# Kernel tuning notes

Hardware: AMD Instinct MI355X
Metric: run time of the kernel (lower is better)

## Reference

```python
import jax, jax.numpy as jnp
import numpy as np

B, T, C = 4, 1024, 1024
H, G = 16, 1            # n_head, n_query_groups
D = C // H              # head_dim = 64
E, K = 4, 1             # moe_num_experts, moe_k
FF = 4 * C              # ffn/expert hidden = 4096
EPS = 1e-5


def setup_inputs() -> dict:
    key = jax.random.key(0)
    ks = jax.random.split(key, 24)
    w = lambda k, shape: (jax.random.normal(k, shape, jnp.float32) * 0.02)
    return {
        "x": jax.random.normal(ks[0], (B, T, C), jnp.float32),
        # attention (torch Linear weights stored as [in, out])
        "wq": w(ks[1], (C, C)), "wk": w(ks[2], (C, C)), "wv": w(ks[3], (C, C)),
        "wo": w(ks[4], (C, C)), "bo": jnp.zeros((C,), jnp.float32),
        # feedforward
        "ff_w1": w(ks[5], (C, FF)), "ff_b1": jnp.zeros((FF,), jnp.float32),
        "ff_w2": w(ks[6], (FF, C)), "ff_b2": jnp.zeros((C,), jnp.float32),
        # MoE experts (stacked) + gate
        "exp_w1": w(ks[7], (E, C, FF)), "exp_b1": jnp.zeros((E, FF), jnp.float32),
        "exp_w2": w(ks[8], (E, FF, C)), "exp_b2": jnp.zeros((E, C), jnp.float32),
        "gate_w": w(ks[9], (C, E)), "gate_b": jnp.zeros((E,), jnp.float32),
        # layernorms
        "ln1_g": jnp.ones((C,), jnp.float32), "ln1_b": jnp.zeros((C,), jnp.float32),
        "ln2_g": jnp.ones((C,), jnp.float32), "ln2_b": jnp.zeros((C,), jnp.float32),
        "ln3_g": jnp.ones((C,), jnp.float32), "ln3_b": jnp.zeros((C,), jnp.float32),
    }


def _ln(x, g, b):
    m = x.mean(-1, keepdims=True)
    v = x.var(-1, keepdims=True)
    return (x - m) / jnp.sqrt(v + EPS) * g + b


def reference(x, wq, wk, wv, wo, bo, ff_w1, ff_b1, ff_w2, ff_b2,
              exp_w1, exp_b1, exp_w2, exp_b2, gate_w, gate_b,
              ln1_g, ln1_b, ln2_g, ln2_b, ln3_g, ln3_b):
    Hg = H // G
    # ---- grouped-query causal self-attention ----
    h = _ln(x, ln1_g, ln1_b)
    # [B,T,C] -> [B,G,Hg,T,D]
    q = (h @ wq).reshape(B, T, G, Hg, D).transpose(0, 2, 3, 1, 4)
    k = (h @ wk).reshape(B, T, G, Hg, D).transpose(0, 2, 3, 1, 4)
    v = (h @ wv).reshape(B, T, G, Hg, D).transpose(0, 2, 3, 1, 4)
    scores = jnp.einsum('bghtd,bghsd->bghts', q, k) / np.float32(np.sqrt(D))
    causal = jnp.tril(jnp.ones((T, T), bool))
    scores = jnp.where(causal, scores, -jnp.inf)
    probs = jax.nn.softmax(scores, axis=-1)
    o = jnp.einsum('bghts,bghsd->bghtd', probs, v)          # [B,G,Hg,T,D]
    o = o.reshape(B, H, T, D).transpose(0, 2, 1, 3).reshape(B, T, C)
    x = x + o @ wo + bo
    # ---- dense feedforward ----
    h = _ln(x, ln2_g, ln2_b)
    x = x + jax.nn.relu(h @ ff_w1 + ff_b1) @ ff_w2 + ff_b2
    # ---- MoE: compute ALL experts densely, gather top-k (faithful to source) ----
    h = _ln(x, ln3_g, ln3_b)
    gate = h @ gate_w + gate_b                               # [B,T,E]
    topk_s, topk_i = jax.lax.top_k(gate, K)                  # [B,T,K]
    topk_w = jax.nn.softmax(topk_s, axis=-1)
    hidden = jax.nn.relu(jnp.einsum('btc,ech->bteh', h, exp_w1) + exp_b1)
    expert_out = jnp.einsum('bteh,ehc->btec', hidden, exp_w2) + exp_b2  # [B,T,E,C]
    sel = jnp.take_along_axis(expert_out, topk_i[..., None], axis=2)    # [B,T,K,C]
    moe = (sel * topk_w[..., None]).sum(axis=2)
    return x + moe
```

## Files before the change

kernel.cpp:

```cpp
#include <hip/hip_runtime.h>


using f16   = _Float16;
using f16x4 = __attribute__((ext_vector_type(4))) _Float16;
using f16x8 = __attribute__((ext_vector_type(8))) _Float16;
using f32x4 = __attribute__((ext_vector_type(4))) float;

__device__ __forceinline__ void async16(void* l, const void* g) {
  __builtin_amdgcn_global_load_lds(
      (const __attribute__((address_space(1))) unsigned*)g,
      (__attribute__((address_space(3))) unsigned*)l, 16, 0, 0);
}

template <bool SPLITW>
__global__ __launch_bounds__(256) void transpose_k(
    const float* __restrict__ in, f16* __restrict__ oh, f16* __restrict__ ol,
    int R, int Cc) {
  const size_t bofs = (size_t)blockIdx.y * R * Cc;
  in += bofs; oh += bofs;
  if constexpr (SPLITW) ol += bofs;
  __shared__ float tile[32][33];
  const int nbx = Cc >> 5;
  const int bx = blockIdx.x % nbx, by = blockIdx.x / nbx;
  const int tx = threadIdx.x & 31, ty = threadIdx.x >> 5;
#pragma unroll
  for (int i = 0; i < 4; ++i) {
    int r = ty + i * 8;
    tile[r][tx] = in[(size_t)(by * 32 + r) * Cc + bx * 32 + tx];
  }
  __syncthreads();
#pragma unroll
  for (int i = 0; i < 4; ++i) {
    int oc = ty + i * 8;
    float v = tile[tx][oc];
    size_t o = (size_t)(bx * 32 + oc) * R + by * 32 + tx;
    f16 hi = (f16)v;
    oh[o] = hi;
    if constexpr (SPLITW) ol[o] = (f16)(v - (float)hi);
  }
}

__global__ __launch_bounds__(256) void ln_k(
    const float* __restrict__ x, const float* __restrict__ g,
    const float* __restrict__ b, f16* __restrict__ outh, f16* __restrict__ outl) {
  const int row = blockIdx.x;
  const float4 vv = ((const float4*)(x + (size_t)row * 1024))[threadIdx.x];
  float s = vv.x + vv.y + vv.z + vv.w;
  float sq = vv.x * vv.x + vv.y * vv.y + vv.z * vv.z + vv.w * vv.w;
#pragma unroll
  for (int mm = 32; mm; mm >>= 1) { s += __shfl_xor(s, mm); sq += __shfl_xor(sq, mm); }
  __shared__ float red[8];
  const int wv = threadIdx.x >> 6;
  if ((threadIdx.x & 63) == 0) { red[wv] = s; red[4 + wv] = sq; }
  __syncthreads();
  s = red[0] + red[1] + red[2] + red[3];
  sq = red[4] + red[5] + red[6] + red[7];
  const float mean = s * 0.0009765625f;
  const float rstd = rsqrtf(sq * 0.0009765625f - mean * mean + 1e-5f);
  const int c = threadIdx.x * 4;
  const float xs[4] = {vv.x, vv.y, vv.z, vv.w};
  f16x4 ovh, ovl;
#pragma unroll
  for (int i = 0; i < 4; ++i) {
    float val = (xs[i] - mean) * rstd * g[c + i] + b[c + i];
    f16 hi = (f16)val;
    ovh[i] = hi;
    ovl[i] = (f16)(val - (float)hi);
  }
  *(f16x4*)(outh + (size_t)row * 1024 + c) = ovh;
  *(f16x4*)(outl + (size_t)row * 1024 + c) = ovl;
}

__global__ __launch_bounds__(256) void gate_k(
    const float* __restrict__ x, const float* __restrict__ g, const float* __restrict__ b,
    const float* __restrict__ gw, const float* __restrict__ gb,
    int* __restrict__ cnt, int* __restrict__ idxAll, int* __restrict__ eid) {
  const int t = blockIdx.x;
  const float4 vv = ((const float4*)(x + (size_t)t * 1024))[threadIdx.x];
  float s = vv.x + vv.y + vv.z + vv.w;
  float sq = vv.x * vv.x + vv.y * vv.y + vv.z * vv.z + vv.w * vv.w;
#pragma unroll
  for (int mm = 32; mm; mm >>= 1) { s += __shfl_xor(s, mm); sq += __shfl_xor(sq, mm); }
  __shared__ float red[8];
  __shared__ float redv[4][4];
  const int wv = threadIdx.x >> 6;
  if ((threadIdx.x & 63) == 0) { red[wv] = s; red[4 + wv] = sq; }
  __syncthreads();
  s = red[0] + red[1] + red[2] + red[3];
  sq = red[4] + red[5] + red[6] + red[7];
  const float mean = s * 0.0009765625f;
  const float rstd = rsqrtf(sq * 0.0009765625f - mean * mean + 1e-5f);
  const int c = threadIdx.x * 4;
  const float xs[4] = {vv.x, vv.y, vv.z, vv.w};
  float a0 = 0.f, a1 = 0.f, a2 = 0.f, a3 = 0.f;
#pragma unroll
  for (int i = 0; i < 4; ++i) {
    float ln = (xs[i] - mean) * rstd * g[c + i] + b[c + i];
    const float4 w4 = ((const float4*)gw)[c + i];
    a0 += ln * w4.x; a1 += ln * w4.y; a2 += ln * w4.z; a3 += ln * w4.w;
  }
#pragma unroll
  for (int mm = 32; mm; mm >>= 1) {
    a0 += __shfl_xor(a0, mm); a1 += __shfl_xor(a1, mm);
    a2 += __shfl_xor(a2, mm); a3 += __shfl_xor(a3, mm);
  }
  if ((threadIdx.x & 63) == 0) {
    redv[wv][0] = a0; redv[wv][1] = a1; redv[wv][2] = a2; redv[wv][3] = a3;
  }
  __syncthreads();
  if (threadIdx.x == 0) {
    float ge[4];
#pragma unroll
    for (int e = 0; e < 4; ++e)
      ge[e] = redv[0][e] + redv[1][e] + redv[2][e] + redv[3][e] + gb[e];
    int be = 0; float bvv = ge[0];
#pragma unroll
    for (int e = 1; e < 4; ++e) if (ge[e] > bvv) { bvv = ge[e]; be = e; }
    int pos = atomicAdd(&cnt[be], 1);
    idxAll[(be << 12) + pos] = t;
    eid[t] = be;
  }
}

__global__ void init_moe(int* cnt) { if (threadIdx.x < 4) cnt[threadIdx.x] = 0; }

#define MAXMT 36
__global__ void plan_k(const int* __restrict__ cnt, int* __restrict__ desc) {
  if (threadIdx.x == 0) {
    int t = 0;
    for (int e = 0; e < 4; ++e) {
      const int c = cnt[e];
      for (int m = 0; m < c; m += 128) desc[t++] = (e << 16) | (m >> 7);
    }
    for (; t < MAXMT; ++t) desc[t] = -1;
  }
}

template <bool MOE>
__global__ __launch_bounds__(256) void reduce_k(
    const float* __restrict__ p0, const float* __restrict__ p1,
    const float* __restrict__ res, const float* __restrict__ bias,
    const int* __restrict__ eid, float* __restrict__ o) {
  const int row = blockIdx.x, t = threadIdx.x;
  const float* bp = MOE ? bias + (size_t)eid[row] * 1024 : bias;
  const float4 a = ((const float4*)(p0 + (size_t)row * 1024))[t];
  const float4 b = ((const float4*)(p1 + (size_t)row * 1024))[t];
  const float4 r = ((const float4*)(res + (size_t)row * 1024))[t];
  const float4 bb = ((const float4*)bp)[t];
  float4 o4;
  o4.x = r.x + a.x + b.x + bb.x;
  o4.y = r.y + a.y + b.y + bb.y;
  o4.z = r.z + a.z + b.z + bb.z;
  o4.w = r.w + a.w + b.w + bb.w;
  ((float4*)(o + (size_t)row * 1024))[t] = o4;
}

template <bool SPLIT, bool RELU, bool BIAS, bool RES, bool GATHER, int OUT,
          bool QKV3, bool KSPLIT>
__global__ __launch_bounds__(256, SPLIT ? 2 : 3) void gemm_k(
    const f16* __restrict__ Ah, const f16* __restrict__ Al,
    const f16* __restrict__ Bh, const f16* __restrict__ Bl,
    float* __restrict__ outf, float* __restrict__ outf2,
    f16* __restrict__ outh, f16* __restrict__ outl,
    const float* __restrict__ bias, const float* __restrict__ res,
    const int* __restrict__ idxAll, const int* __restrict__ cntAll,
    const int* __restrict__ desc,
    int M, int N, int K) {
  const int NB = N >> 7;
  int m0, n0, ks = 0;
  int cnt = M;
  const int* idx = nullptr;
  if constexpr (GATHER) {
    int rem = blockIdx.x;
    if constexpr (KSPLIT) {
      const int half = (int)gridDim.x >> 1;
      ks = rem >= half; rem -= ks * half;
    }
    const int mt = rem / NB, nt = rem - mt * NB;
    const int d = desc[mt];
    if (d < 0) return;
    const int e = d >> 16;
    m0 = (d & 0xffff) << 7;
    n0 = nt << 7;
    cnt = cntAll[e];
    idx = idxAll + (e << 12);
    Bh += (size_t)e * N * K;
    if constexpr (SPLIT) Bl += (size_t)e * N * K;
    if (BIAS) bias += (size_t)e * N;
  } else {
    int rem = blockIdx.x;
    const int ntile = (int)gridDim.x >> (KSPLIT ? 1 : 0);
    if constexpr (KSPLIT) { ks = rem >= ntile; rem -= ks * ntile; }
    const int q2 = ntile >> 3;
    const int bid = (rem & 7) * q2 + (rem >> 3);
    m0 = (bid / NB) << 7; n0 = (bid % NB) << 7;
  }

  constexpr int RB = SPLIT ? 32768 : 16384;
  __shared__ __align__(16) char lds[SPLIT ? 65536 : 32768];

  const int tid = threadIdx.x;
  const int wave = tid >> 6, lane = tid & 63;
  const int wr = (wave >> 1) << 6, wc = (wave & 1) << 6;
  const int srow = lane >> 3;
  const int lc = (lane & 7) ^ srow;
  const int kofs = lc << 4;

  const int kshift = (KSPLIT && ks) ? (K >> 1) : 0;

  const char* sAh[4];
  const char* sAl[4];
  const char* sBh[4];
  const char* sBl[4];
#pragma unroll
  for (int s = 0; s < 4; ++s) {
    const int tr = (wave * 4 + s) * 8 + srow;
    int gm = m0 + tr;
    if constexpr (GATHER) gm = idx[gm < cnt ? gm : cnt - 1];
    sAh[s] = (const char*)Ah + ((size_t)gm * K + kshift) * 2 + kofs;
    sBh[s] = (const char*)Bh + ((size_t)(n0 + tr) * K + kshift) * 2 + kofs;
    if constexpr (SPLIT) {
      sAl[s] = (const char*)Al + ((size_t)gm * K + kshift) * 2 + kofs;
      sBl[s] = (const char*)Bl + ((size_t)(n0 + tr) * K + kshift) * 2 + kofs;
    }
  }
  char* const dstw = lds + wave * 4096;

  const int s4 = lane >> 4, l7 = lane & 7, fr = lane & 15;
  int rowA[4], colB[4];
#pragma unroll
  for (int i = 0; i < 4; ++i) rowA[i] = (wr + i * 16 + fr) * 128;
#pragma unroll
  for (int j = 0; j < 4; ++j) colB[j] = RB + (wc + j * 16 + fr) * 128;
  const int ch[2] = {((s4) ^ l7) << 4, ((4 + s4) ^ l7) << 4};

  f32x4 acc[4][4] = {};

  const int nt_ = (KSPLIT ? (K >> 1) : K) >> 6;

  for (int t = 0; t < nt_; ++t) {
    const size_t kb = (size_t)t << 7;
#pragma unroll
    for (int s = 0; s < 4; ++s) {
      async16(dstw + s * 1024, sAh[s] + kb);
      if constexpr (SPLIT) async16(dstw + 16384 + s * 1024, sAl[s] + kb);
      async16(dstw + RB + s * 1024, sBh[s] + kb);
      if constexpr (SPLIT) async16(dstw + RB + 16384 + s * 1024, sBl[s] + kb);
    }
    __syncthreads();
    __builtin_amdgcn_s_setprio(1);
#pragma unroll
    for (int kk = 0; kk < 2; ++kk) {
      f16x8 va[4], vb[4], va2[4], vb2[4];
#pragma unroll
      for (int i = 0; i < 4; ++i) {
        va[i] = *(const f16x8*)(lds + rowA[i] + ch[kk]);
        if constexpr (SPLIT) va2[i] = *(const f16x8*)(lds + 16384 + rowA[i] + ch[kk]);
      }
#pragma unroll
      for (int j = 0; j < 4; ++j) {
        vb[j] = *(const f16x8*)(lds + colB[j] + ch[kk]);
        if constexpr (SPLIT) vb2[j] = *(const f16x8*)(lds + 16384 + colB[j] + ch[kk]);
      }
#pragma unroll
      for (int i = 0; i < 4; ++i)
#pragma unroll
        for (int j = 0; j < 4; ++j) {
          acc[i][j] = __builtin_amdgcn_mfma_f32_16x16x32_f16(va[i], vb[j], acc[i][j], 0, 0, 0);
          if constexpr (SPLIT) {
            acc[i][j] = __builtin_amdgcn_mfma_f32_16x16x32_f16(va2[i], vb[j], acc[i][j], 0, 0, 0);
            acc[i][j] = __builtin_amdgcn_mfma_f32_16x16x32_f16(va[i], vb2[j], acc[i][j], 0, 0, 0);
          }
        }
    }
    __builtin_amdgcn_s_setprio(0);
    __syncthreads();
  }

  const int cl = lane & 15, rg = lane >> 4;
  float* const po = (OUT == 3) ? (ks ? outf2 : outf) : outf;
#pragma unroll
  for (int i = 0; i < 4; ++i) {
#pragma unroll
    for (int r = 0; r < 4; ++r) {
      const int mloc = m0 + wr + i * 16 + rg * 4 + r;
      if (GATHER && mloc >= cnt) continue;
      const int orow = GATHER ? idx[mloc] : mloc;
#pragma unroll
      for (int j = 0; j < 4; ++j) {
        const int col = n0 + wc + j * 16 + cl;
        float v2 = acc[i][j][r];
        if (BIAS) v2 += bias[col];
        if (RELU) v2 = v2 > 0.f ? v2 : 0.f;
        if (RES) v2 += res[(size_t)orow * N + col];
        size_t oidx;
        if constexpr (QKV3) {
          if (col < 2048) {
            oidx = ((size_t)(col >> 10) * M + orow) * 1024 + (col & 1023);
          } else {
            const int c = col - 2048;
            oidx = (size_t)2 * M * 1024 +
                   (((size_t)(orow >> 10) * 16 + (c >> 6)) * 64 + (c & 63)) * 1024 +
                   (orow & 1023);
          }
        } else {
          oidx = (size_t)orow * N + col;
        }
        if constexpr (OUT == 0 || OUT == 3) {
          po[oidx] = v2;
        } else if constexpr (OUT == 1) {
          f16 hi = (f16)v2;
          outh[oidx] = hi;
          outl[oidx] = (f16)(v2 - (float)hi);
        } else {
          outh[oidx] = (f16)v2;
        }
      }
    }
  }
}

__global__ __launch_bounds__(256, 3) void attn_k(
    const f16* __restrict__ qh, const f16* __restrict__ ql,
    const f16* __restrict__ kh, const f16* __restrict__ kl,
    const f16* __restrict__ vth, const f16* __restrict__ vtl,
    f16* __restrict__ oh, f16* __restrict__ ol) {
  const int qt = 15 - (blockIdx.x & 15), hd = (blockIdx.x >> 4) & 15, bb = blockIdx.x >> 8;
  const int tid = threadIdx.x, wave = tid >> 6, lane = tid & 63;
  __shared__ __align__(16) char QPs[16384], Ks[16384], Vs[16384];
  const int swz = (((lane & 7) ^ ((lane >> 3) & 7)) << 4);
  const size_t tok0 = (size_t)bb * 1024;
  const int hoff = hd * 64;
  const size_t vbase = ((size_t)(bb * 16 + hd) * 64) * 1024;
  const float L2E = 1.44269504089f;

#pragma unroll
  for (int r = 0; r < 2; ++r) {
    const int chunk = wave * 2 + r;
    const int row = chunk * 8 + (lane >> 3);
    const size_t byte = (((tok0 + qt * 64 + row) * 1024 + hoff) << 1) + swz;
    async16(QPs + chunk * 1024, (const char*)qh + byte);
    async16(QPs + 8192 + chunk * 1024, (const char*)ql + byte);
  }
  __syncthreads();
  f16x8 qr_h[2], qr_l[2];
#pragma unroll
  for (int ks = 0; ks < 2; ++ks) {
    const int qrow = wave * 16 + (lane & 15);
    const int qoff = qrow * 128 + ((((ks << 2) + (lane >> 4)) ^ (qrow & 7)) << 4);
    qr_h[ks] = *(const f16x8*)(QPs + qoff);
    qr_l[ks] = *(const f16x8*)(QPs + 8192 + qoff);
  }

  f32x4 oacc[4] = {};
  float mrun[4] = {-1e30f, -1e30f, -1e30f, -1e30f};
  float lrun[4] = {};

  for (int kt = 0; kt <= qt; ++kt) {
    __syncthreads();
#pragma unroll
    for (int r = 0; r < 2; ++r) {
      const int chunk = wave * 2 + r;
      const int row = chunk * 8 + (lane >> 3);
      const size_t kbyte = (((tok0 + kt * 64 + row) * 1024 + hoff) << 1) + swz;
      async16(Ks + chunk * 1024, (const char*)kh + kbyte);
      async16(Ks + 8192 + chunk * 1024, (const char*)kl + kbyte);
      const size_t vbyte = (((vbase + (size_t)row * 1024) + kt * 64) << 1) + swz;
      async16(Vs + chunk * 1024, (const char*)vth + vbyte);
      async16(Vs + 8192 + chunk * 1024, (const char*)vtl + vbyte);
    }
    __syncthreads();

    f32x4 s[4] = {};
#pragma unroll
    for (int ks = 0; ks < 2; ++ks) {
#pragma unroll
      for (int j = 0; j < 4; ++j) {
        const int col = j * 16 + (lane & 15);
        const int koff = col * 128 + ((((ks << 2) + (lane >> 4)) ^ (col & 7)) << 4);
        f16x8 b_h = *(const f16x8*)(Ks + koff);
        f16x8 b_l = *(const f16x8*)(Ks + 8192 + koff);
        s[j] = __builtin_amdgcn_mfma_f32_16x16x32_f16(qr_h[ks], b_h, s[j], 0, 0, 0);
        s[j] = __builtin_amdgcn_mfma_f32_16x16x32_f16(qr_l[ks], b_h, s[j], 0, 0, 0);
        s[j] = __builtin_amdgcn_mfma_f32_16x16x32_f16(qr_h[ks], b_l, s[j], 0, 0, 0);
      }
    }

    const bool diag = (kt == qt);
    float pmax[4] = {-1e30f, -1e30f, -1e30f, -1e30f};
#pragma unroll
    for (int j = 0; j < 4; ++j)
#pragma unroll
      for (int r = 0; r < 4; ++r) {
        float sv = s[j][r] * 0.125f;
        if (diag) {
          const int qloc = wave * 16 + (lane >> 4) * 4 + r;
          const int kvl = j * 16 + (lane & 15);
          if (kvl > qloc) sv = -1e30f;
        }
        s[j][r] = sv;
        pmax[r] = fmaxf(pmax[r], sv);
      }
    char* pbh = QPs + wave * 2048;
    char* pbl = QPs + 8192 + wave * 2048;
#pragma unroll
    for (int r = 0; r < 4; ++r) {
#pragma unroll
      for (int mm = 1; mm < 16; mm <<= 1)
        pmax[r] = fmaxf(pmax[r], __shfl_xor(pmax[r], mm, 16));
      const float mnew = fmaxf(mrun[r], pmax[r]);
      const float al = exp2f((mrun[r] - mnew) * L2E);
      mrun[r] = mnew;
      lrun[r] *= al;
      oacc[0][r] *= al; oacc[1][r] *= al; oacc[2][r] *= al; oacc[3][r] *= al;
    }

    float psum[4] = {};
#pragma unroll
    for (int j = 0; j < 4; ++j)
#pragma unroll
      for (int r = 0; r < 4; ++r) {
        const float p = exp2f((s[j][r] - mrun[r]) * L2E);
        psum[r] += p;
        const int lr = (lane >> 4) * 4 + r;
        const int kvl = j * 16 + (lane & 15);
        const int poff = lr * 128 + ((kvl * 2) ^ ((lr & 7) << 4));
        f16 ph = (f16)p;
        *(f16*)(pbh + poff) = ph;
        *(f16*)(pbl + poff) = (f16)(p - (float)ph);
      }
#pragma unroll
    for (int r = 0; r < 4; ++r) {
#pragma unroll
      for (int mm = 1; mm < 16; mm <<= 1)
        psum[r] += __shfl_xor(psum[r], mm, 16);
      lrun[r] += psum[r];
    }

#pragma unroll
    for (int ks = 0; ks < 2; ++ks) {
      const int prow = lane & 15;
      const int poff = prow * 128 + ((((ks << 2) + (lane >> 4)) ^ (prow & 7)) << 4);
      f16x8 a_h = *(const f16x8*)(pbh + poff);
      f16x8 a_l = *(const f16x8*)(pbl + poff);
#pragma unroll
      for (int jd = 0; jd < 4; ++jd) {
        const int col = jd * 16 + (lane & 15);
        const int voff = col * 128 + ((((ks << 2) + (lane >> 4)) ^ (col & 7)) << 4);
        f16x8 b_h = *(const f16x8*)(Vs + voff);
        f16x8 b_l = *(const f16x8*)(Vs + 8192 + voff);
        oacc[jd] = __builtin_amdgcn_mfma_f32_16x16x32_f16(a_h, b_h, oacc[jd], 0, 0, 0);
        oacc[jd] = __builtin_amdgcn_mfma_f32_16x16x32_f16(a_l, b_h, oacc[jd], 0, 0, 0);
        oacc[jd] = __builtin_amdgcn_mfma_f32_16x16x32_f16(a_h, b_l, oacc[jd], 0, 0, 0);
      }
    }
  }

#pragma unroll
  for (int r = 0; r < 4; ++r) {
    const float inv = 1.0f / lrun[r];
    const size_t trow = tok0 + qt * 64 + wave * 16 + (lane >> 4) * 4 + r;
#pragma unroll
    for (int jd = 0; jd < 4; ++jd) {
      const int col = hoff + jd * 16 + (lane & 15);
      const float val = oacc[jd][r] * inv;
      const f16 hi = (f16)val;
      oh[trow * 1024 + col] = hi;
      ol[trow * 1024 + col] = (f16)(val - (float)hi);
    }
  }
}

extern "C" void kernel_launch(void* const* d_in, const int* in_sizes, int n_in,
                              void* d_out, int out_size, void* d_ws, size_t ws_size,
                              hipStream_t stream) {
  const float* x0   = (const float*)d_in[0];
  const float* wq   = (const float*)d_in[1];
  const float* wk   = (const float*)d_in[2];
  const float* wv   = (const float*)d_in[3];
  const float* wo   = (const float*)d_in[4];
  const float* bo   = (const float*)d_in[5];
  const float* ffw1 = (const float*)d_in[6];
  const float* ffb1 = (const float*)d_in[7];
  const float* ffw2 = (const float*)d_in[8];
  const float* ffb2 = (const float*)d_in[9];
  const float* ew1  = (const float*)d_in[10];
  const float* eb1  = (const float*)d_in[11];
  const float* ew2  = (const float*)d_in[12];
  const float* eb2  = (const float*)d_in[13];
  const float* gw   = (const float*)d_in[14];
  const float* gb   = (const float*)d_in[15];
  const float* l1g  = (const float*)d_in[16];
  const float* l1b  = (const float*)d_in[17];
  const float* l2g  = (const float*)d_in[18];
  const float* l2b  = (const float*)d_in[19];
  const float* l3g  = (const float*)d_in[20];
  const float* l3b  = (const float*)d_in[21];
  float* out = (float*)d_out;

  char* w = (char*)d_ws;
  const size_t M1 = (size_t)1024 * 1024;
  const size_t A1 = (size_t)4096 * 1024 * 2;
  const size_t W4 = (size_t)1024 * 4096 * 2;
  f16* wqkvh = (f16*)w; w += 3 * M1 * 2;
  f16* wqkvl = (f16*)w; w += 3 * M1 * 2;
  f16* woh = (f16*)w; w += M1 * 2;
  f16* wol = (f16*)w; w += M1 * 2;
  f16* f1h = (f16*)w; w += W4;  f16* f1l = (f16*)w; w += W4;
  f16* f2h = (f16*)w; w += W4;  f16* f2l = (f16*)w; w += W4;
  f16* e1t = (f16*)w; w += 4 * W4;
  f16* e2t = (f16*)w; w += 4 * W4;
  f16* hh  = (f16*)w; w += A1;  f16* hl  = (f16*)w; w += A1;
  f16* qkv_h = (f16*)w; w += 3 * A1;
  f16* qkv_l = (f16*)w; w += 3 * A1;
  f16* o_h = (f16*)w; w += A1;  f16* o_l = (f16*)w; w += A1;
  float* x1 = (float*)w; w += (size_t)4096 * 1024 * 4;
  int* cnt = (int*)w; w += 256;
  int* idx = (int*)w; w += (size_t)4 * 4096 * 4;
  int* eid = (int*)w; w += (size_t)4096 * 4;
  int* desc = (int*)w; w += 256;
  f16* hid_h = qkv_h;
  f16* hid_l = (f16*)((char*)qkv_h + (((size_t)32) << 20));
  f16* ffh   = qkv_h;
  float* pW0 = (float*)hh;
  float* pW1 = (float*)qkv_h;
  float* pF0 = (float*)wqkvh;
  float* pF1 = (float*)hh;
  float* pM0 = (float*)((char*)qkv_l + (((size_t)8) << 20));
  float* pM1 = (float*)o_h;

  transpose_k<true><<<1024, 256, 0, stream>>>(wq, wqkvh, wqkvl, 1024, 1024);
  transpose_k<true><<<1024, 256, 0, stream>>>(wk, wqkvh + M1, wqkvl + M1, 1024, 1024);
  transpose_k<true><<<1024, 256, 0, stream>>>(wv, wqkvh + 2 * M1, wqkvl + 2 * M1, 1024, 1024);
  transpose_k<true><<<1024, 256, 0, stream>>>(wo, woh, wol, 1024, 1024);
  transpose_k<true><<<4096, 256, 0, stream>>>(ffw1, f1h, f1l, 1024, 4096);
  transpose_k<true><<<4096, 256, 0, stream>>>(ffw2, f2h, f2l, 4096, 1024);
  transpose_k<false><<<dim3(4096, 4), 256, 0, stream>>>(ew1, e1t, nullptr, 1024, 4096);
  transpose_k<false><<<dim3(4096, 4), 256, 0, stream>>>(ew2, e2t, nullptr, 4096, 1024);

  const size_t TOK = (size_t)4096 * 1024;
  ln_k<<<4096, 256, 0, stream>>>(x0, l1g, l1b, hh, hl);
  gemm_k<true, false, false, false, false, 1, true, false><<<768, 256, 0, stream>>>(
      hh, hl, wqkvh, wqkvl, nullptr, nullptr, qkv_h, qkv_l,
      nullptr, nullptr, nullptr, nullptr, nullptr, 4096, 3072, 1024);
  attn_k<<<1024, 256, 0, stream>>>(qkv_h, qkv_l, qkv_h + TOK, qkv_l + TOK,
                                   qkv_h + 2 * TOK, qkv_l + 2 * TOK, o_h, o_l);
  gemm_k<true, false, false, false, false, 3, false, true><<<512, 256, 0, stream>>>(
      o_h, o_l, woh, wol, pW0, pW1, nullptr, nullptr,
      nullptr, nullptr, nullptr, nullptr, nullptr, 4096, 1024, 1024);
  reduce_k<false><<<4096, 256, 0, stream>>>(pW0, pW1, x0, bo, nullptr, x1);

  ln_k<<<4096, 256, 0, stream>>>(x1, l2g, l2b, hh, hl);
  gemm_k<true, true, true, false, false, 1, false, false><<<1024, 256, 0, stream>>>(
      hh, hl, f1h, f1l, nullptr, nullptr, hid_h, hid_l,
      ffb1, nullptr, nullptr, nullptr, nullptr, 4096, 4096, 1024);
  gemm_k<true, false, false, false, false, 3, false, true><<<512, 256, 0, stream>>>(
      hid_h, hid_l, f2h, f2l, pF0, pF1, nullptr, nullptr,
      nullptr, nullptr, nullptr, nullptr, nullptr, 4096, 1024, 4096);
  reduce_k<false><<<4096, 256, 0, stream>>>(pF0, pF1, x1, ffb2, nullptr, out);

  ln_k<<<4096, 256, 0, stream>>>(out, l3g, l3b, hh, hl);
  init_moe<<<1, 64, 0, stream>>>(cnt);
  gate_k<<<4096, 256, 0, stream>>>(out, l3g, l3b, gw, gb, cnt, idx, eid);
  plan_k<<<1, 64, 0, stream>>>(cnt, desc);
  gemm_k<false, true, true, false, true, 2, false, false><<<MAXMT * 32, 256, 0, stream>>>(
      hh, nullptr, e1t, nullptr, nullptr, nullptr, ffh, nullptr,
      eb1, nullptr, idx, cnt, desc, 4096, 4096, 1024);
  gemm_k<false, false, false, false, true, 3, false, true><<<2 * MAXMT * 8, 256, 0, stream>>>(
      ffh, nullptr, e2t, nullptr, pM0, pM1, nullptr, nullptr,
      nullptr, nullptr, idx, cnt, desc, 4096, 1024, 4096);
  reduce_k<true><<<4096, 256, 0, stream>>>(pM0, pM1, out, eb2, eid, out);
}
```

Before: 730.9 us.

## Use 256x256 GEMM tiles with 512 threads, double-buffered LDS and 4-way K-split

Rewrites the GEMM kernel to use 256x256 output tiles computed by 8 waves. LDS is double-buffered (128KB), so the global-to-LDS load of the next K tile overlaps the MFMA work on the current one. The split-fp16 path becomes three sequential passes over K (hi*hi, lo*hi, hi*lo) instead of three interleaved MFMAs. Output-projection and down-projection GEMMs now split K four ways, with a wider reduce kernel summing four partials, and partial buffers are remapped onto scratch regions plus one new buffer. The intent is more data reuse per tile and better latency hiding, at the cost of one block per CU, fewer blocks in the grid, coarser MoE tile padding, and more partial-sum traffic.

```diff
diff --git a/kernel.cpp b/kernel.cpp
--- a/kernel.cpp
+++ b/kernel.cpp
@@ -124,13 +124,13 @@
 
 __global__ void init_moe(int* cnt) { if (threadIdx.x < 4) cnt[threadIdx.x] = 0; }
 
-#define MAXMT 36
+#define MAXMT 20
 __global__ void plan_k(const int* __restrict__ cnt, int* __restrict__ desc) {
   if (threadIdx.x == 0) {
     int t = 0;
     for (int e = 0; e < 4; ++e) {
       const int c = cnt[e];
-      for (int m = 0; m < c; m += 128) desc[t++] = (e << 16) | (m >> 7);
+      for (int m = 0; m < c; m += 256) desc[t++] = (e << 16) | (m >> 8);
     }
     for (; t < MAXMT; ++t) desc[t] = -1;
   }
@@ -139,49 +139,53 @@
 template <bool MOE>
 __global__ __launch_bounds__(256) void reduce_k(
     const float* __restrict__ p0, const float* __restrict__ p1,
+    const float* __restrict__ p2, const float* __restrict__ p3,
     const float* __restrict__ res, const float* __restrict__ bias,
     const int* __restrict__ eid, float* __restrict__ o) {
   const int row = blockIdx.x, t = threadIdx.x;
   const float* bp = MOE ? bias + (size_t)eid[row] * 1024 : bias;
   const float4 a = ((const float4*)(p0 + (size_t)row * 1024))[t];
   const float4 b = ((const float4*)(p1 + (size_t)row * 1024))[t];
+  const float4 c = ((const float4*)(p2 + (size_t)row * 1024))[t];
+  const float4 d = ((const float4*)(p3 + (size_t)row * 1024))[t];
   const float4 r = ((const float4*)(res + (size_t)row * 1024))[t];
   const float4 bb = ((const float4*)bp)[t];
   float4 o4;
-  o4.x = r.x + a.x + b.x + bb.x;
-  o4.y = r.y + a.y + b.y + bb.y;
-  o4.z = r.z + a.z + b.z + bb.z;
-  o4.w = r.w + a.w + b.w + bb.w;
+  o4.x = r.x + a.x + b.x + c.x + d.x + bb.x;
+  o4.y = r.y + a.y + b.y + c.y + d.y + bb.y;
+  o4.z = r.z + a.z + b.z + c.z + d.z + bb.z;
+  o4.w = r.w + a.w + b.w + c.w + d.w + bb.w;
   ((float4*)(o + (size_t)row * 1024))[t] = o4;
 }
 
 template <bool SPLIT, bool RELU, bool BIAS, bool RES, bool GATHER, int OUT,
-          bool QKV3, bool KSPLIT>
-__global__ __launch_bounds__(256, SPLIT ? 2 : 3) void gemm_k(
+          bool QKV3, int KS>
+__global__ __launch_bounds__(512, 1) void gemm_k(
     const f16* __restrict__ Ah, const f16* __restrict__ Al,
     const f16* __restrict__ Bh, const f16* __restrict__ Bl,
-    float* __restrict__ outf, float* __restrict__ outf2,
+    float* __restrict__ p0, float* __restrict__ p1,
+    float* __restrict__ p2, float* __restrict__ p3,
     f16* __restrict__ outh, f16* __restrict__ outl,
     const float* __restrict__ bias, const float* __restrict__ res,
     const int* __restrict__ idxAll, const int* __restrict__ cntAll,
     const int* __restrict__ desc,
     int M, int N, int K) {
-  const int NB = N >> 7;
+  const int NB = N >> 8;
   int m0, n0, ks = 0;
   int cnt = M;
   const int* idx = nullptr;
   if constexpr (GATHER) {
     int rem = blockIdx.x;
-    if constexpr (KSPLIT) {
-      const int half = (int)gridDim.x >> 1;
-      ks = rem >= half; rem -= ks * half;
+    if constexpr (KS > 1) {
+      const int per = (int)gridDim.x / KS;
+      ks = rem / per; rem -= ks * per;
     }
     const int mt = rem / NB, nt = rem - mt * NB;
     const int d = desc[mt];
     if (d < 0) return;
     const int e = d >> 16;
-    m0 = (d & 0xffff) << 7;
-    n0 = nt << 7;
+    m0 = (d & 0xffff) << 8;
+    n0 = nt << 8;
     cnt = cntAll[e];
     idx = idxAll + (e << 12);
     Bh += (size_t)e * N * K;
@@ -189,106 +193,118 @@
     if (BIAS) bias += (size_t)e * N;
   } else {
     int rem = blockIdx.x;
-    const int ntile = (int)gridDim.x >> (KSPLIT ? 1 : 0);
-    if constexpr (KSPLIT) { ks = rem >= ntile; rem -= ks * ntile; }
-    const int q2 = ntile >> 3;
-    const int bid = (rem & 7) * q2 + (rem >> 3);
-    m0 = (bid / NB) << 7; n0 = (bid % NB) << 7;
-  }
-
-  constexpr int RB = SPLIT ? 32768 : 16384;
-  __shared__ __align__(16) char lds[SPLIT ? 65536 : 32768];
+    const int ntile = (int)gridDim.x / KS;
+    if constexpr (KS > 1) { ks = rem / ntile; rem -= ks * ntile; }
+    const int q = ntile >> 3;
+    const int bid = (rem & 7) * q + (rem >> 3);
+    m0 = (bid / NB) << 8; n0 = (bid % NB) << 8;
+  }
+
+  __shared__ __align__(16) char lds[131072];
 
   const int tid = threadIdx.x;
   const int wave = tid >> 6, lane = tid & 63;
-  const int wr = (wave >> 1) << 6, wc = (wave & 1) << 6;
-  const int srow = lane >> 3;
-  const int lc = (lane & 7) ^ srow;
-  const int kofs = lc << 4;
-
-  const int kshift = (KSPLIT && ks) ? (K >> 1) : 0;
-
-  const char* sAh[4];
-  const char* sAl[4];
-  const char* sBh[4];
-  const char* sBl[4];
+  const int wm = wave >> 2, wn = wave & 3;
+  const int srow = lane >> 3, l7 = lane & 7;
+  const int kofs = (l7 ^ srow) << 4;
+
+  const int Kp = K / KS;
+  const int kshift = ks * Kp;
+  const int ntk = Kp >> 6;
+  const int nt = SPLIT ? 3 * ntk : ntk;
+
+  unsigned offA[4], offB[4];
 #pragma unroll
   for (int s = 0; s < 4; ++s) {
-    const int tr = (wave * 4 + s) * 8 + srow;
-    int gm = m0 + tr;
+    const int ar = wave * 32 + s * 8 + srow;
+    int gm = m0 + ar;
     if constexpr (GATHER) gm = idx[gm < cnt ? gm : cnt - 1];
-    sAh[s] = (const char*)Ah + ((size_t)gm * K + kshift) * 2 + kofs;
-    sBh[s] = (const char*)Bh + ((size_t)(n0 + tr) * K + kshift) * 2 + kofs;
+    offA[s] = (unsigned)(((size_t)gm * K + kshift) * 2) + kofs;
+    offB[s] = (unsigned)(((size_t)(n0 + ar) * K + kshift) * 2) + kofs;
+  }
+
+  const char* const baseAh = (const char*)Ah;
+  const char* const baseAl = (const char*)Al;
+  const char* const baseBh = (const char*)Bh;
+  const char* const baseBl = (const char*)Bl;
+
+  auto stage = [&](int tile, int buf) {
+    int p = 0, kt = tile;
     if constexpr (SPLIT) {
-      sAl[s] = (const char*)Al + ((size_t)gm * K + kshift) * 2 + kofs;
-      sBl[s] = (const char*)Bl + ((size_t)(n0 + tr) * K + kshift) * 2 + kofs;
-    }
-  }
-  char* const dstw = lds + wave * 4096;
-
-  const int s4 = lane >> 4, l7 = lane & 7, fr = lane & 15;
-  int rowA[4], colB[4];
-#pragma unroll
-  for (int i = 0; i < 4; ++i) rowA[i] = (wr + i * 16 + fr) * 128;
-#pragma unroll
-  for (int j = 0; j < 4; ++j) colB[j] = RB + (wc + j * 16 + fr) * 128;
-  const int ch[2] = {((s4) ^ l7) << 4, ((4 + s4) ^ l7) << 4};
-
-  f32x4 acc[4][4] = {};
-
-  const int nt_ = (KSPLIT ? (K >> 1) : K) >> 6;
-
-  for (int t = 0; t < nt_; ++t) {
-    const size_t kb = (size_t)t << 7;
+      p = (tile >= 2 * ntk) ? 2 : (tile >= ntk ? 1 : 0);
+      kt = tile - p * ntk;
+    }
+    const char* bA = (SPLIT && p == 1) ? baseAl : baseAh;
+    const char* bB = (SPLIT && p == 2) ? baseBl : baseBh;
+    const unsigned kb = (unsigned)kt << 7;
+    char* dst = lds + buf * 65536 + wave * 4096;
 #pragma unroll
     for (int s = 0; s < 4; ++s) {
-      async16(dstw + s * 1024, sAh[s] + kb);
-      if constexpr (SPLIT) async16(dstw + 16384 + s * 1024, sAl[s] + kb);
-      async16(dstw + RB + s * 1024, sBh[s] + kb);
-      if constexpr (SPLIT) async16(dstw + RB + 16384 + s * 1024, sBl[s] + kb);
-    }
-    __syncthreads();
+      async16(dst + s * 1024, bA + offA[s] + kb);
+      async16(dst + 32768 + s * 1024, bB + offB[s] + kb);
+    }
+  };
+
+  const int s4 = lane >> 4, fr = lane & 15;
+  int roA[8], roB[4];
+#pragma unroll
+  for (int i = 0; i < 8; ++i) roA[i] = (wm * 128 + i * 16 + fr) * 128;
+#pragma unroll
+  for (int j = 0; j < 4; ++j) roB[j] = 32768 + (wn * 64 + j * 16 + fr) * 128;
+  const int ch0 = (s4 ^ l7) << 4;
+  const int ch1 = ((4 + s4) ^ l7) << 4;
+
+  f32x4 acc[8][4] = {};
+
+  stage(0, 0);
+  __syncthreads();
+
+  for (int t = 0; t < nt; ++t) {
+    const char* cb = lds + (t & 1) * 65536;
+    f16x8 a[8], b[4];
+#pragma unroll
+    for (int i = 0; i < 8; ++i) a[i] = *(const f16x8*)(cb + roA[i] + ch0);
+#pragma unroll
+    for (int j = 0; j < 4; ++j) b[j] = *(const f16x8*)(cb + roB[j] + ch0);
+    if (t + 1 < nt) stage(t + 1, (t + 1) & 1);
     __builtin_amdgcn_s_setprio(1);
 #pragma unroll
-    for (int kk = 0; kk < 2; ++kk) {
-      f16x8 va[4], vb[4], va2[4], vb2[4];
-#pragma unroll
-      for (int i = 0; i < 4; ++i) {
-        va[i] = *(const f16x8*)(lds + rowA[i] + ch[kk]);
-        if constexpr (SPLIT) va2[i] = *(const f16x8*)(lds + 16384 + rowA[i] + ch[kk]);
-      }
-#pragma unroll
-      for (int j = 0; j < 4; ++j) {
-        vb[j] = *(const f16x8*)(lds + colB[j] + ch[kk]);
-        if constexpr (SPLIT) vb2[j] = *(const f16x8*)(lds + 16384 + colB[j] + ch[kk]);
-      }
-#pragma unroll
-      for (int i = 0; i < 4; ++i)
-#pragma unroll
-        for (int j = 0; j < 4; ++j) {
-          acc[i][j] = __builtin_amdgcn_mfma_f32_16x16x32_f16(va[i], vb[j], acc[i][j], 0, 0, 0);
-          if constexpr (SPLIT) {
-            acc[i][j] = __builtin_amdgcn_mfma_f32_16x16x32_f16(va2[i], vb[j], acc[i][j], 0, 0, 0);
-            acc[i][j] = __builtin_amdgcn_mfma_f32_16x16x32_f16(va[i], vb2[j], acc[i][j], 0, 0, 0);
-          }
-        }
-    }
+    for (int i = 0; i < 8; ++i)
+#pragma unroll
+      for (int j = 0; j < 4; ++j)
+        acc[i][j] = __builtin_amdgcn_mfma_f32_16x16x32_f16(a[i], b[j], acc[i][j], 0, 0, 0);
+    __builtin_amdgcn_s_setprio(0);
+#pragma unroll
+    for (int i = 0; i < 8; ++i) a[i] = *(const f16x8*)(cb + roA[i] + ch1);
+#pragma unroll
+    for (int j = 0; j < 4; ++j) b[j] = *(const f16x8*)(cb + roB[j] + ch1);
+    __builtin_amdgcn_s_setprio(1);
+#pragma unroll
+    for (int i = 0; i < 8; ++i)
+#pragma unroll
+      for (int j = 0; j < 4; ++j)
+        acc[i][j] = __builtin_amdgcn_mfma_f32_16x16x32_f16(a[i], b[j], acc[i][j], 0, 0, 0);
     __builtin_amdgcn_s_setprio(0);
     __syncthreads();
   }
 
   const int cl = lane & 15, rg = lane >> 4;
-  float* const po = (OUT == 3) ? (ks ? outf2 : outf) : outf;
-#pragma unroll
-  for (int i = 0; i < 4; ++i) {
+  float* po;
+  if constexpr (OUT == 3) {
+    po = (ks == 0) ? p0 : (ks == 1) ? p1 : (ks == 2) ? p2 : p3;
+  } else {
+    po = p0;
+  }
+#pragma unroll
+  for (int i = 0; i < 8; ++i) {
 #pragma unroll
     for (int r = 0; r < 4; ++r) {
-      const int mloc = m0 + wr + i * 16 + rg * 4 + r;
+      const int mloc = m0 + wm * 128 + i * 16 + rg * 4 + r;
       if (GATHER && mloc >= cnt) continue;
       const int orow = GATHER ? idx[mloc] : mloc;
 #pragma unroll
       for (int j = 0; j < 4; ++j) {
-        const int col = n0 + wc + j * 16 + cl;
+        const int col = n0 + wn * 64 + j * 16 + cl;
         float v2 = acc[i][j][r];
         if (BIAS) v2 += bias[col];
         if (RELU) v2 = v2 > 0.f ? v2 : 0.f;
@@ -515,6 +531,7 @@
   f16* qkv_l = (f16*)w; w += 3 * A1;
   f16* o_h = (f16*)w; w += A1;  f16* o_l = (f16*)w; w += A1;
   float* x1 = (float*)w; w += (size_t)4096 * 1024 * 4;
+  float* extraP = (float*)w; w += (size_t)4096 * 1024 * 4;
   int* cnt = (int*)w; w += 256;
   int* idx = (int*)w; w += (size_t)4 * 4096 * 4;
   int* eid = (int*)w; w += (size_t)4096 * 4;
@@ -522,12 +539,19 @@
   f16* hid_h = qkv_h;
   f16* hid_l = (f16*)((char*)qkv_h + (((size_t)32) << 20));
   f16* ffh   = qkv_h;
-  float* pW0 = (float*)hh;
-  float* pW1 = (float*)qkv_h;
-  float* pF0 = (float*)wqkvh;
-  float* pF1 = (float*)hh;
-  float* pM0 = (float*)((char*)qkv_l + (((size_t)8) << 20));
-  float* pM1 = (float*)o_h;
+  const size_t MB16 = ((size_t)16) << 20;
+  float* wP0 = (float*)qkv_h;
+  float* wP1 = (float*)((char*)qkv_h + MB16);
+  float* wP2 = (float*)((char*)qkv_h + 2 * MB16);
+  float* wP3 = (float*)hh;
+  float* fP0 = (float*)wqkvh;
+  float* fP1 = (float*)f1h;
+  float* fP2 = (float*)hh;
+  float* fP3 = extraP;
+  float* mP0 = (float*)hh;
+  float* mP1 = (float*)o_h;
+  float* mP2 = x1;
+  float* mP3 = extraP;
 
   transpose_k<true><<<1024, 256, 0, stream>>>(wq, wqkvh, wqkvl, 1024, 1024);
   transpose_k<true><<<1024, 256, 0, stream>>>(wk, wqkvh + M1, wqkvl + M1, 1024, 1024);
@@ -540,34 +564,34 @@
 
   const size_t TOK = (size_t)4096 * 1024;
   ln_k<<<4096, 256, 0, stream>>>(x0, l1g, l1b, hh, hl);
-  gemm_k<true, false, false, false, false, 1, true, false><<<768, 256, 0, stream>>>(
-      hh, hl, wqkvh, wqkvl, nullptr, nullptr, qkv_h, qkv_l,
+  gemm_k<true, false, false, false, false, 1, true, 1><<<192, 512, 0, stream>>>(
+      hh, hl, wqkvh, wqkvl, nullptr, nullptr, nullptr, nullptr, qkv_h, qkv_l,
       nullptr, nullptr, nullptr, nullptr, nullptr, 4096, 3072, 1024);
   attn_k<<<1024, 256, 0, stream>>>(qkv_h, qkv_l, qkv_h + TOK, qkv_l + TOK,
                                    qkv_h + 2 * TOK, qkv_l + 2 * TOK, o_h, o_l);
-  gemm_k<true, false, false, false, false, 3, false, true><<<512, 256, 0, stream>>>(
-      o_h, o_l, woh, wol, pW0, pW1, nullptr, nullptr,
+  gemm_k<true, false, false, false, false, 3, false, 4><<<256, 512, 0, stream>>>(
+      o_h, o_l, woh, wol, wP0, wP1, wP2, wP3, nullptr, nullptr,
       nullptr, nullptr, nullptr, nullptr, nullptr, 4096, 1024, 1024);
-  reduce_k<false><<<4096, 256, 0, stream>>>(pW0, pW1, x0, bo, nullptr, x1);
+  reduce_k<false><<<4096, 256, 0, stream>>>(wP0, wP1, wP2, wP3, x0, bo, nullptr, x1);
 
   ln_k<<<4096, 256, 0, stream>>>(x1, l2g, l2b, hh, hl);
-  gemm_k<true, true, true, false, false, 1, false, false><<<1024, 256, 0, stream>>>(
-      hh, hl, f1h, f1l, nullptr, nullptr, hid_h, hid_l,
+  gemm_k<true, true, true, false, false, 1, false, 1><<<256, 512, 0, stream>>>(
+      hh, hl, f1h, f1l, nullptr, nullptr, nullptr, nullptr, hid_h, hid_l,
       ffb1, nullptr, nullptr, nullptr, nullptr, 4096, 4096, 1024);
-  gemm_k<true, false, false, false, false, 3, false, true><<<512, 256, 0, stream>>>(
-      hid_h, hid_l, f2h, f2l, pF0, pF1, nullptr, nullptr,
+  gemm_k<true, false, false, false, false, 3, false, 4><<<256, 512, 0, stream>>>(
+      hid_h, hid_l, f2h, f2l, fP0, fP1, fP2, fP3, nullptr, nullptr,
       nullptr, nullptr, nullptr, nullptr, nullptr, 4096, 1024, 4096);
-  reduce_k<false><<<4096, 256, 0, stream>>>(pF0, pF1, x1, ffb2, nullptr, out);
+  reduce_k<false><<<4096, 256, 0, stream>>>(fP0, fP1, fP2, fP3, x1, ffb2, nullptr, out);
 
   ln_k<<<4096, 256, 0, stream>>>(out, l3g, l3b, hh, hl);
   init_moe<<<1, 64, 0, stream>>>(cnt);
   gate_k<<<4096, 256, 0, stream>>>(out, l3g, l3b, gw, gb, cnt, idx, eid);
   plan_k<<<1, 64, 0, stream>>>(cnt, desc);
-  gemm_k<false, true, true, false, true, 2, false, false><<<MAXMT * 32, 256, 0, stream>>>(
-      hh, nullptr, e1t, nullptr, nullptr, nullptr, ffh, nullptr,
+  gemm_k<false, true, true, false, true, 2, false, 1><<<MAXMT * 16, 512, 0, stream>>>(
+      hh, nullptr, e1t, nullptr, nullptr, nullptr, nullptr, nullptr, ffh, nullptr,
       eb1, nullptr, idx, cnt, desc, 4096, 4096, 1024);
-  gemm_k<false, false, false, false, true, 3, false, true><<<2 * MAXMT * 8, 256, 0, stream>>>(
-      ffh, nullptr, e2t, nullptr, pM0, pM1, nullptr, nullptr,
+  gemm_k<false, false, false, false, true, 3, false, 4><<<4 * MAXMT * 4, 512, 0, stream>>>(
+      ffh, nullptr, e2t, nullptr, mP0, mP1, mP2, mP3, nullptr, nullptr,
       nullptr, nullptr, idx, cnt, desc, 4096, 1024, 4096);
-  reduce_k<true><<<4096, 256, 0, stream>>>(pM0, pM1, out, eb2, eid, out);
-}
+  reduce_k<true><<<4096, 256, 0, stream>>>(mP0, mP1, mP2, mP3, out, eb2, eid, out);
+}
```

Result: slower. 781.7 us (+6.9%).
